# Performance work log

Measured on AMD Instinct MI355X. Metric: run time of the kernel, lower is better.

## Reference

```python
import jax, jax.numpy as jnp
import numpy as np


def _glorot(key, shape):
    lim = np.sqrt(6.0 / (shape[-2] + shape[-1])).astype(np.float32)
    return jax.random.uniform(key, shape, jnp.float32, -lim, lim)


def setup_inputs() -> dict:
    key = jax.random.key(0)
    B, F, K, L = 8192, 256, 32768, 4
    H = 2 * F          # CouplingLayer(feat_size, feat_size * 2) hidden width
    half = F // 2      # affine coupling transforms half the features
    ks = jax.random.split(key, 6)
    return {
        "inputs": jax.random.normal(ks[0], (B, F), jnp.float32),
        "W1": _glorot(ks[1], (L, half, H)),
        "b1": jnp.zeros((L, H), jnp.float32),
        "Ws": _glorot(ks[2], (L, H, half)),
        "bs": jnp.zeros((L, half), jnp.float32),
        "Wt": _glorot(ks[3], (L, H, half)),
        "bt": jnp.zeros((L, half), jnp.float32),
        "prior": _glorot(ks[4], (K, F)),  # VQ codebook, GlorotUniform init as in source
    }


def _forward_flow(x, W1, b1, Ws, bs, Wt, bt):
    """Stack of affine coupling layers; returns (y, log|det J|) per sample."""
    L = W1.shape[0]
    jac = jnp.zeros((x.shape[0],), x.dtype)
    for l in range(L):  # small fixed layer count
        xa, xb = jnp.split(x, 2, axis=1)                 # [B, F/2] each
        h = jax.nn.relu(xa @ W1[l] + b1[l])              # [B, 2F]
        s_raw = h @ Ws[l] + bs[l]                        # [B, F/2]
        s = s_raw if l == L - 1 else jnp.tanh(s_raw)     # last layer: tf.identity
        t = h @ Wt[l] + bt[l]
        yb = xb * jnp.exp(s) + t
        jac = jac + jnp.sum(s, axis=1)
        x = jnp.concatenate([yb, xa], axis=1)            # swap halves for mixing
    return x, jac


def reference(inputs, W1, b1, Ws, bs, Wt, bt, prior):
    sg = jax.lax.stop_gradient
    x, jac = _forward_flow(inputs, W1, b1, Ws, bs, Wt, bt)   # [B, F], [B]
    # pairwise squared distance to codebook: [B, K]
    na = jnp.sum(x * x, axis=1, keepdims=True)               # [B, 1]
    nb = jnp.sum(prior * prior, axis=1)[None, :]             # [1, K]
    d = jnp.maximum(na - 2.0 * (x @ prior.T) + nb, 0.0)      # [B, K]
    target_ind = jnp.argmin(d, axis=1)                       # [B]
    target = prior[target_ind]                               # gather, [B, F]
    loss_1 = jnp.mean(jnp.sum((x - sg(target)) ** 2, axis=1) / 2)
    loss_2 = jnp.mean(jnp.sum((sg(x) - target) ** 2, axis=1) / 2)
    loss = loss_1 + 0.25 * loss_2 - jnp.mean(jac)
    return x, loss
```

## Files before the change

### kernel.cpp

```cpp
#include <hip/hip_runtime.h>
#include <hip/hip_fp8.h>
#include <stdint.h>

#define NB     8192
#define NF     256
#define NHALF  128
#define NHID   512
#define NLAY   4
#define NK     32768

#define SX     (1.0f / 16.0f)
#define SP     (256.0f)

typedef __attribute__((ext_vector_type(8))) short bf16x8;
typedef __attribute__((ext_vector_type(4))) float f32x4;
typedef __attribute__((ext_vector_type(2))) long i64x2;

static __device__ __forceinline__ unsigned short f2bf(float f) {
  union { float f; unsigned int u; } v; v.f = f;
  return (unsigned short)((v.u + 0x7FFFu + ((v.u >> 16) & 1u)) >> 16);
}
static __device__ __forceinline__ float bf2f(unsigned short u) {
  union { unsigned int u; float f; } v; v.u = ((unsigned int)u) << 16; return v.f;
}
static __device__ __forceinline__ unsigned char f2fp8(float f) {
  __hip_fp8_e4m3 q(f);
  return (unsigned char)q.__x;
}
static __device__ __forceinline__ float fp82f(unsigned char b) {
  __hip_fp8_e4m3 q; q.__x = b; return (float)q;
}
static __device__ __forceinline__ int kperm(int k) {
  return ((k >> 3) & 3) * 64 + ((k >> 5) << 3) + (k & 7);
}

static __device__ __forceinline__ void load_lds16(const void* g, void* l) {
  __builtin_amdgcn_global_load_lds(
      (const __attribute__((address_space(1))) unsigned int*)g,
      (__attribute__((address_space(3))) unsigned int*)l, 16, 0, 0);
}

static __device__ __forceinline__ unsigned long long packsi(float v, int idx) {
  unsigned int b = __float_as_uint(v);
  b = (b & 0x80000000u) ? ~b : (b | 0x80000000u);
  return ((unsigned long long)b << 32) | (unsigned int)(~(unsigned int)idx);
}

static __device__ __forceinline__ float fast_tanh(float x) {
  const float xc = fminf(fmaxf(x, -15.f), 15.f);
  const float e2 = __expf(2.f * xc);
  return 1.f - 2.f / (e2 + 1.f);
}

static __device__ __forceinline__ int swadr(int kseg, int nrows, int row, int kin) {
  return (kseg * nrows + row) * 64 + (((kin >> 3) ^ (row & 7)) * 8) + (kin & 7);
}

static __device__ __forceinline__ void stage_seg(
    int g, unsigned short* dst,
    const unsigned short* __restrict__ W1T,
    const unsigned short* __restrict__ W2I,
    int wave, int lane)
{
  const int l = g / 24, s = g % 24, nc = s / 3, t = s % 3;
  if (t == 0) {
    const unsigned short* W1l = W1T + (size_t)l * (NHID * NHALF) + (size_t)nc * 64 * 128;
#pragma unroll
    for (int u = 0; u < 4; u++) {
      const int chb = (u * 4 + wave) * 64;
      const int ch = chb + lane;
      const int kseg = ch >> 9, cs = ch & 511;
      const int row = cs >> 3, cc = (cs & 7) ^ (row & 7);
      load_lds16(W1l + (size_t)row * 128 + kseg * 64 + cc * 8, dst + chb * 8);
    }
  } else {
    const unsigned short* W2l = W2I + (size_t)l * (NF * NHID) + nc * 64 + (t - 1) * 32;
#pragma unroll
    for (int u = 0; u < 4; u++) {
      const int chb = (u * 4 + wave) * 64;
      const int ch = chb + lane;
      const int row = ch >> 2;
      const int cc = (ch & 3) ^ ((row >> 1) & 3);
      load_lds16(W2l + (size_t)row * NHID + cc * 8, dst + chb * 8);
    }
  }
}

__global__ __launch_bounds__(256, 2)
void flow_all(const float* __restrict__ in,
              const unsigned short* __restrict__ W1T,
              const unsigned short* __restrict__ W2I,
              const float* __restrict__ b1A,
              const float* __restrict__ bsA,
              const float* __restrict__ btA,
              float* __restrict__ xout,
              unsigned char* __restrict__ xf8,
              float* __restrict__ jac)
{
  __shared__ __align__(16) unsigned short Xb[2][16 * 128];
  __shared__ __align__(16) unsigned short Hs[16 * 64];
  __shared__ __align__(16) unsigned short Bs[3][8192];
  __shared__ float b1s[NLAY * NHID];
  __shared__ float bss[NLAY * NHALF];
  __shared__ float bts[NLAY * NHALF];
  __shared__ float jlds[3][16];
  const int tid = threadIdx.x;
  const int lane = tid & 63, wave = tid >> 6;
  const int q = lane >> 4, c = lane & 15;
  const int m0 = blockIdx.x * 16;

  stage_seg(0, Bs[0], W1T, W2I, wave, lane);

#pragma unroll
  for (int v = 0; v < 4; v++) {
    const int t4 = tid + v * 256;
    const int row = t4 >> 6, f4 = t4 & 63;
    const float4 d = *(const float4*)(in + (size_t)(m0 + row) * NF + f4 * 4);
    unsigned short* dst = Xb[f4 >> 5];
    const int feat = (f4 & 31) * 4;
    const float vals[4] = {d.x, d.y, d.z, d.w};
#pragma unroll
    for (int u = 0; u < 4; u++) {
      const int fe = feat + u;
      dst[swadr(fe >> 6, 16, row, fe & 63)] = f2bf(vals[u]);
    }
  }

#pragma unroll
  for (int v = 0; v < 8; v++) b1s[tid + v * 256] = b1A[tid + v * 256];
#pragma unroll
  for (int v = 0; v < 2; v++) {
    bss[tid + v * 256] = bsA[tid + v * 256];
    bts[tid + v * 256] = btA[tid + v * 256];
  }

  stage_seg(1, Bs[1], W1T, W2I, wave, lane);

  float jr[4] = {0.f, 0.f, 0.f, 0.f};
  bf16x8 af1[4];
  const f32x4 z = {0.f, 0.f, 0.f, 0.f};
  f32x4 acc2[4];

  for (int gs = 0; gs < 96; gs++) {
    if (gs < 95)
      asm volatile("s_waitcnt vmcnt(4) lgkmcnt(0)\n\ts_barrier" ::: "memory");
    else
      asm volatile("s_waitcnt vmcnt(0) lgkmcnt(0)\n\ts_barrier" ::: "memory");

    if (gs + 2 < 96) stage_seg(gs + 2, Bs[(gs + 2) % 3], W1T, W2I, wave, lane);

    const int l = gs / 24, s = gs % 24, nc8 = s / 3, typ = s % 3;
    const unsigned short* B = Bs[gs % 3];
    unsigned short* XA = Xb[l & 1];
    unsigned short* XB = Xb[1 - (l & 1)];

    if (typ == 0) {
      if (s == 0) {
#pragma unroll
        for (int kw = 0; kw < 4; kw++) {
          const int kch = kw * 4 + q;
          af1[kw] = *(const bf16x8*)(XA + ((kch >> 3) * 16 + c) * 64 +
                                     (((kch & 7) ^ (c & 7)) * 8));
        }
#pragma unroll
        for (int j = 0; j < 4; j++) acc2[j] = z;
      }
      f32x4 acc1 = z;
      const int rb = wave * 16 + c;
#pragma unroll
      for (int kw = 0; kw < 4; kw++) {
        const int kseg = kw >> 1, g = (kw & 1) * 4 + q;
        const bf16x8 bf = *(const bf16x8*)(B + (kseg * 64 + rb) * 64 + ((g ^ (rb & 7)) * 8));
        acc1 = __builtin_amdgcn_mfma_f32_16x16x32_bf16(af1[kw], bf, acc1, 0, 0, 0);
      }
      const int hc = wave * 16 + c;
      const float bb = b1s[l * NHID + nc8 * 64 + hc];
#pragma unroll
      for (int r = 0; r < 4; r++) {
        float v = acc1[r] + bb;
        v = v > 0.f ? v : 0.f;
        Hs[swadr(0, 16, 4 * q + r, hc)] = f2bf(v);
      }
    } else {
      const int half = typ - 1;
      const bf16x8 afh = *(const bf16x8*)(Hs + c * 64 + (((half * 4 + q) ^ (c & 7)) * 8));
#pragma unroll
      for (int j = 0; j < 4; j++) {
        const int rb = wave * 64 + 16 * j + c;
        const bf16x8 bf = *(const bf16x8*)(B + rb * 32 + ((q ^ ((rb >> 1) & 3)) * 8));
        acc2[j] = __builtin_amdgcn_mfma_f32_16x16x32_bf16(afh, bf, acc2[j], 0, 0, 0);
      }
    }

    if (s == 23) {
      const int parity = c & 1;
      const int lastl = (l == NLAY - 1);
      const float* bsl = bss + l * NHALF;
      const float* btl = bts + l * NHALF;
#pragma unroll
      for (int j = 0; j < 4; j++) {
        const int col = wave * 64 + 16 * j + c;
#pragma unroll
        for (int r = 0; r < 4; r++) {
          const float val = acc2[j][r];
          const float oth = __shfl_xor(val, 1);
          if (!parity) {
            const int feat = col >> 1;
            float sv = val + bsl[feat];
            if (!lastl) sv = fast_tanh(sv);
            const float t = oth + btl[feat];
            const int row = 4 * q + r;
            const int xaddr = swadr(feat >> 6, 16, row, feat & 63);
            const float xb = bf2f(XB[xaddr]);
            const float yb = xb * __expf(sv) + t;
            jr[r] += sv;
            XB[xaddr] = f2bf(yb);
            if (l >= 2) {
              const int k = lastl ? feat : (NHALF + feat);
              const size_t grow = (size_t)(m0 + row) * NF;
              xout[grow + k] = yb;
              xf8[(size_t)(m0 + row) * 256 + kperm(k)] = f2fp8(yb * SX);
            }
          }
        }
      }
    }
  }

  float v0[4];
#pragma unroll
  for (int r = 0; r < 4; r++) {
    float v = jr[r];
    v += __shfl_xor(v, 1); v += __shfl_xor(v, 2);
    v += __shfl_xor(v, 4); v += __shfl_xor(v, 8);
    if (c == 0) {
      if (wave) jlds[wave - 1][4 * q + r] = v;
      else v0[r] = v;
    }
  }
  __syncthreads();
  if (wave == 0 && c == 0) {
#pragma unroll
    for (int r = 0; r < 4; r++) {
      const int row = 4 * q + r;
      jac[m0 + row] = v0[r] + jlds[0][row] + jlds[1][row] + jlds[2][row];
    }
  }
}

__global__ __launch_bounds__(256, 2)
void vq_argmax(const unsigned char* __restrict__ X8,
               const unsigned char* __restrict__ P8,
               const float* __restrict__ nbh,
               unsigned long long* __restrict__ gbest)
{
  __shared__ __align__(16) unsigned char Bs[2][64 * 256];
  const int tid = threadIdx.x;
  const int lane = tid & 63, wave = tid >> 6;
  const int y = blockIdx.x & 15;
  const int m0 = (blockIdx.x >> 4) * 256;
  const int q = lane >> 4, c = lane & 15;
  const int mw = m0 + wave * 64;

  long af[4][8];
#pragma unroll
  for (int i = 0; i < 4; i++) {
    const unsigned char* xr = X8 + (size_t)(mw + 16 * i + c) * 256 + q * 64;
#pragma unroll
    for (int kc2 = 0; kc2 < 4; kc2++) {
      const i64x2 v = *(const i64x2*)(xr + kc2 * 16);
      af[i][2 * kc2] = v.x; af[i][2 * kc2 + 1] = v.y;
    }
  }

  float bestv[16];
  int besti[16];
#pragma unroll
  for (int t = 0; t < 16; t++) { bestv[t] = -1e30f; besti[t] = 0; }

  {
    const int n0s = y * 2048;
#pragma unroll
    for (int u = 0; u < 4; u++) {
      const int chb = (u * 4 + wave) * 64;
      const int ch = chb + lane;
      const int row = ch >> 4, gslot = ch & 15;
      load_lds16(P8 + (size_t)(n0s + row) * 256 + (gslot ^ (row & 15)) * 16,
                 Bs[0] + chb * 16);
    }
  }

  for (int nt = 0; nt < 32; nt++) {
    const int n0 = y * 2048 + nt * 64;
    __syncthreads();

    float nbr[4];
#pragma unroll
    for (int j = 0; j < 4; j++) nbr[j] = nbh[n0 + 16 * j + c];

    if (nt + 1 < 32) {
      const int n0s = n0 + 64;
      unsigned char* dst = Bs[(nt + 1) & 1];
#pragma unroll
      for (int u = 0; u < 4; u++) {
        const int chb = (u * 4 + wave) * 64;
        const int ch = chb + lane;
        const int row = ch >> 4, gslot = ch & 15;
        load_lds16(P8 + (size_t)(n0s + row) * 256 + (gslot ^ (row & 15)) * 16,
                   dst + chb * 16);
      }
    }

    const unsigned char* Bt = Bs[nt & 1];
    const f32x4 z = {0.f, 0.f, 0.f, 0.f};
    f32x4 acc[4][4];
#pragma unroll
    for (int i = 0; i < 4; i++)
#pragma unroll
      for (int j = 0; j < 4; j++) acc[i][j] = z;

#pragma unroll
    for (int kc2 = 0; kc2 < 4; kc2++) {
      const int g = q * 4 + kc2;
#pragma unroll
      for (int j = 0; j < 4; j++) {
        const int rb = 16 * j + c;
        const i64x2 b2 = *(const i64x2*)(Bt + rb * 256 + ((g ^ (rb & 15)) * 16));
#pragma unroll
        for (int i = 0; i < 4; i++) {
          acc[i][j] = __builtin_amdgcn_mfma_f32_16x16x32_fp8_fp8(af[i][2 * kc2],     b2.x, acc[i][j], 0, 0, 0);
          acc[i][j] = __builtin_amdgcn_mfma_f32_16x16x32_fp8_fp8(af[i][2 * kc2 + 1], b2.y, acc[i][j], 0, 0, 0);
        }
      }
    }

#pragma unroll
    for (int j = 0; j < 4; j++) {
      const int col = n0 + 16 * j + c;
      const float nb = nbr[j];
#pragma unroll
      for (int i = 0; i < 4; i++)
#pragma unroll
        for (int r = 0; r < 4; r++) {
          const float sc = acc[i][j][r] - nb;
          const int t = i * 4 + r;
          if (sc > bestv[t]) { bestv[t] = sc; besti[t] = col; }
        }
    }
  }

#pragma unroll
  for (int t = 0; t < 16; t++) {
    float lv = bestv[t]; int li = besti[t];
#pragma unroll
    for (int mk = 8; mk >= 1; mk >>= 1) {
      const float ov = __shfl_xor(lv, mk);
      const int oi = __shfl_xor(li, mk);
      if (ov > lv || (ov == lv && oi < li)) { lv = ov; li = oi; }
    }
    if (c == 0) {
      const int row = mw + 16 * (t >> 2) + q * 4 + (t & 3);
      atomicMax(&gbest[row], packsi(lv, li));
    }
  }
}

__global__ void prep_all(const float* __restrict__ W1,
                         const float* __restrict__ Ws,
                         const float* __restrict__ Wt,
                         const float* __restrict__ prior,
                         unsigned short* __restrict__ W1T,
                         unsigned short* __restrict__ W2I,
                         unsigned char* __restrict__ p8,
                         float* __restrict__ nbh,
                         unsigned long long* __restrict__ gbest,
                         float* __restrict__ accum)
{
  __shared__ float ts[64 * 65];
  const int bx = blockIdx.x;
  const int tid = threadIdx.x;
  if (bx < 2048) {
    const int k = bx * 16 + (tid >> 4);
    const int l16 = tid & 15;
    float s = 0.f;
#pragma unroll
    for (int v = 0; v < 4; v++) {
      const int off = (v * 16 + l16) * 4;
      const float4 d = *(const float4*)(prior + (size_t)k * NF + off);
      uchar4 o;
      o.x = f2fp8(d.x * SP); o.y = f2fp8(d.y * SP);
      o.z = f2fp8(d.z * SP); o.w = f2fp8(d.w * SP);
      *(uchar4*)(p8 + (size_t)k * 256 + kperm(off)) = o;
      const float q0 = fp82f(o.x), q1 = fp82f(o.y), q2 = fp82f(o.z), q3 = fp82f(o.w);
      s += q0 * q0 + q1 * q1 + q2 * q2 + q3 * q3;
    }
#pragma unroll
    for (int mk = 8; mk >= 1; mk >>= 1) s += __shfl_xor(s, mk);
    if (l16 == 0) nbh[k] = 0.5f * s * (SX / SP);
  } else if (bx < 2112) {
    const int job = bx - 2048;
    const int l = job >> 4, t = job & 15;
    const int k0 = (t >> 3) * 64, n0 = (t & 7) * 64;
    const float* src = W1 + (size_t)l * NHALF * NHID;
#pragma unroll
    for (int v = 0; v < 16; v++) {
      const int e = tid + v * 256;
      const int kk = e >> 6, nn = e & 63;
      ts[kk * 65 + nn] = src[(size_t)(k0 + kk) * NHID + n0 + nn];
    }
    __syncthreads();
    unsigned short* dst = W1T + (size_t)l * NHID * NHALF;
#pragma unroll
    for (int v = 0; v < 16; v++) {
      const int e = tid + v * 256;
      const int nn = e >> 6, kk = e & 63;
      dst[(size_t)(n0 + nn) * NHALF + k0 + kk] = f2bf(ts[kk * 65 + nn]);
    }
  } else if (bx < 2240) {
    const int job = bx - 2112;
    const int l = job >> 5, rem = job & 31;
    const int b = rem >> 4;
    const int k0 = ((rem >> 1) & 7) * 64;
    const int f0 = (rem & 1) * 64;
    const float* src = (b ? Wt : Ws) + (size_t)l * NHID * NHALF;
#pragma unroll
    for (int v = 0; v < 16; v++) {
      const int e = tid + v * 256;
      const int kk = e >> 6, nn = e & 63;
      ts[kk * 65 + nn] = src[(size_t)(k0 + kk) * NHALF + f0 + nn];
    }
    __syncthreads();
#pragma unroll
    for (int v = 0; v < 16; v++) {
      const int e = tid + v * 256;
      const int nn = e >> 6, kk = e & 63;
      W2I[((size_t)l * NF + 2 * (f0 + nn) + b) * NHID + k0 + kk] = f2bf(ts[kk * 65 + nn]);
    }
  } else {
    const int idx = (bx - 2240) * 256 + tid;
    if (idx < NB) gbest[idx] = 0ull;
    if (idx < 4) accum[idx] = 0.f;
  }
}

__global__ void vq_finalize(const float* __restrict__ X,
                            const float* __restrict__ prior,
                            const unsigned long long* __restrict__ gbest,
                            const float* __restrict__ jac,
                            float* __restrict__ accum,
                            float* __restrict__ loss)
{
  const int wave = threadIdx.x >> 6, lane = threadIdx.x & 63;
  const int gw = blockIdx.x * 4 + wave;
  float accd = 0.f, accj = 0.f;
  for (int r = 0; r < 8; r++) {
    const int row = gw * 8 + r;
    const unsigned int idx = ~(unsigned int)(gbest[row]);
    const float* x = X + (size_t)row * NF;
    const float* p = prior + (size_t)idx * NF;
#pragma unroll
    for (int u = 0; u < 4; u++) {
      const int d = lane + u * 64;
      const float df = x[d] - p[d];
      accd += df * df;
    }
    if (lane == 0) accj += jac[row];
  }
#pragma unroll
  for (int mk = 32; mk >= 1; mk >>= 1) {
    accd += __shfl_xor(accd, mk);
    accj += __shfl_xor(accj, mk);
  }
  __shared__ float sd[4], sj[4];
  if (lane == 0) { sd[wave] = accd; sj[wave] = accj; }
  __syncthreads();
  if (threadIdx.x == 0) {
    atomicAdd(&accum[0], sd[0] + sd[1] + sd[2] + sd[3]);
    atomicAdd(&accum[1], sj[0] + sj[1] + sj[2] + sj[3]);
    __threadfence();
    const unsigned int t = atomicAdd((unsigned int*)&accum[2], 1u);
    if (t == 255u) {
      const float d = atomicAdd(&accum[0], 0.f);
      const float jv = atomicAdd(&accum[1], 0.f);
      loss[0] = 1.25f * (0.5f * d / (float)NB) - jv / (float)NB;
    }
  }
}

extern "C" void kernel_launch(void* const* d_in, const int* in_sizes, int n_in,
                              void* d_out, int out_size, void* d_ws, size_t ws_size,
                              hipStream_t stream)
{
  (void)in_sizes; (void)n_in; (void)out_size; (void)ws_size;
  const float* inputs = (const float*)d_in[0];
  const float* W1 = (const float*)d_in[1];
  const float* b1 = (const float*)d_in[2];
  const float* Ws = (const float*)d_in[3];
  const float* bs = (const float*)d_in[4];
  const float* Wt = (const float*)d_in[5];
  const float* bt = (const float*)d_in[6];
  const float* prior = (const float*)d_in[7];

  char* p = (char*)d_ws;
  auto alloc = [&](size_t bytes) { char* r = p; p += (bytes + 255) & ~(size_t)255; return r; };
  unsigned short* W1T  = (unsigned short*)alloc((size_t)NLAY * NHID * NHALF * 2);
  unsigned short* W2I  = (unsigned short*)alloc((size_t)NLAY * NF * NHID * 2);
  unsigned char* P8    = (unsigned char*)alloc((size_t)NK * 256);
  float* NBH           = (float*)alloc((size_t)NK * 4);
  unsigned char* XF8   = (unsigned char*)alloc((size_t)NB * 256);
  float* JAC           = (float*)alloc((size_t)NB * 4);
  unsigned long long* GBEST = (unsigned long long*)alloc((size_t)NB * 8);
  float* ACC           = (float*)alloc(256);

  float* xout = (float*)d_out;
  float* loss = xout + (size_t)NB * NF;

  prep_all<<<dim3(2272), 256, 0, stream>>>(
      W1, Ws, Wt, prior, W1T, W2I, P8, NBH, GBEST, ACC);

  flow_all<<<dim3(NB / 16), 256, 0, stream>>>(
      inputs, W1T, W2I, b1, bs, bt, xout, XF8, JAC);

  vq_argmax<<<dim3(32 * 16), 256, 0, stream>>>(XF8, P8, NBH, GBEST);
  vq_finalize<<<dim3(256), 256, 0, stream>>>(xout, prior, GBEST, JAC, ACC, loss);
}
```

Measured before the change: 285.7 us.

## Use scaled 16x16x128 fp8 MFMA for codebook distances and stagger weight segments

The codebook distance GEMM moves from the 16x16x32 fp8 MFMA (two per 16-byte load) to the gfx950 scaled 16x16x128 f8f6f4 MFMA with unit scales. That cuts the MFMA instruction count fourfold, and the fp8 layouts of activations and codebook drop the kperm permutation so they match the new operand layout. The negated codebook norm is folded into the accumulator init, removing one subtract per score. Separately, each flow block rotates the order of its hidden-chunk segments and swaps the output halves by block index, spreading concurrent weight reads across addresses. The risks are a wrong operand layout or scale encoding for the new instruction, which would silently change argmin results.

```diff
diff --git a/kernel.cpp b/kernel.cpp
--- a/kernel.cpp
+++ b/kernel.cpp
@@ -14,7 +14,7 @@
 
 typedef __attribute__((ext_vector_type(8))) short bf16x8;
 typedef __attribute__((ext_vector_type(4))) float f32x4;
-typedef __attribute__((ext_vector_type(2))) long i64x2;
+typedef __attribute__((ext_vector_type(8))) int i32x8;
 
 static __device__ __forceinline__ unsigned short f2bf(float f) {
   union { float f; unsigned int u; } v; v.f = f;
@@ -29,9 +29,6 @@
 }
 static __device__ __forceinline__ float fp82f(unsigned char b) {
   __hip_fp8_e4m3 q; q.__x = b; return (float)q;
-}
-static __device__ __forceinline__ int kperm(int k) {
-  return ((k >> 3) & 3) * 64 + ((k >> 5) << 3) + (k & 7);
 }
 
 static __device__ __forceinline__ void load_lds16(const void* g, void* l) {
@@ -60,9 +57,11 @@
     int g, unsigned short* dst,
     const unsigned short* __restrict__ W1T,
     const unsigned short* __restrict__ W2I,
-    int wave, int lane)
+    int wave, int lane, int bxr, int hswap)
 {
-  const int l = g / 24, s = g % 24, nc = s / 3, t = s % 3;
+  const int l = g / 24, s = g % 24;
+  const int nc = ((s / 3) + bxr) & 7;
+  const int t = s % 3;
   if (t == 0) {
     const unsigned short* W1l = W1T + (size_t)l * (NHID * NHALF) + (size_t)nc * 64 * 128;
 #pragma unroll
@@ -74,7 +73,8 @@
       load_lds16(W1l + (size_t)row * 128 + kseg * 64 + cc * 8, dst + chb * 8);
     }
   } else {
-    const unsigned short* W2l = W2I + (size_t)l * (NF * NHID) + nc * 64 + (t - 1) * 32;
+    const int half = (t - 1) ^ hswap;
+    const unsigned short* W2l = W2I + (size_t)l * (NF * NHID) + nc * 64 + half * 32;
 #pragma unroll
     for (int u = 0; u < 4; u++) {
       const int chb = (u * 4 + wave) * 64;
@@ -108,8 +108,10 @@
   const int lane = tid & 63, wave = tid >> 6;
   const int q = lane >> 4, c = lane & 15;
   const int m0 = blockIdx.x * 16;
-
-  stage_seg(0, Bs[0], W1T, W2I, wave, lane);
+  const int bxr = blockIdx.x & 7;
+  const int hswap = (blockIdx.x >> 3) & 1;
+
+  stage_seg(0, Bs[0], W1T, W2I, wave, lane, bxr, hswap);
 
 #pragma unroll
   for (int v = 0; v < 4; v++) {
@@ -134,7 +136,7 @@
     bts[tid + v * 256] = btA[tid + v * 256];
   }
 
-  stage_seg(1, Bs[1], W1T, W2I, wave, lane);
+  stage_seg(1, Bs[1], W1T, W2I, wave, lane, bxr, hswap);
 
   float jr[4] = {0.f, 0.f, 0.f, 0.f};
   bf16x8 af1[4];
@@ -147,9 +149,10 @@
     else
       asm volatile("s_waitcnt vmcnt(0) lgkmcnt(0)\n\ts_barrier" ::: "memory");
 
-    if (gs + 2 < 96) stage_seg(gs + 2, Bs[(gs + 2) % 3], W1T, W2I, wave, lane);
-
-    const int l = gs / 24, s = gs % 24, nc8 = s / 3, typ = s % 3;
+    if (gs + 2 < 96) stage_seg(gs + 2, Bs[(gs + 2) % 3], W1T, W2I, wave, lane, bxr, hswap);
+
+    const int l = gs / 24, s = gs % 24, typ = s % 3;
+    const int nc8 = ((s / 3) + bxr) & 7;
     const unsigned short* B = Bs[gs % 3];
     unsigned short* XA = Xb[l & 1];
     unsigned short* XB = Xb[1 - (l & 1)];
@@ -182,7 +185,7 @@
         Hs[swadr(0, 16, 4 * q + r, hc)] = f2bf(v);
       }
     } else {
-      const int half = typ - 1;
+      const int half = (typ - 1) ^ hswap;
       const bf16x8 afh = *(const bf16x8*)(Hs + c * 64 + (((half * 4 + q) ^ (c & 7)) * 8));
 #pragma unroll
       for (int j = 0; j < 4; j++) {
@@ -219,7 +222,7 @@
               const int k = lastl ? feat : (NHALF + feat);
               const size_t grow = (size_t)(m0 + row) * NF;
               xout[grow + k] = yb;
-              xf8[(size_t)(m0 + row) * 256 + kperm(k)] = f2fp8(yb * SX);
+              xf8[(size_t)(m0 + row) * 256 + k] = f2fp8(yb * SX);
             }
           }
         }
@@ -261,15 +264,17 @@
   const int m0 = (blockIdx.x >> 4) * 256;
   const int q = lane >> 4, c = lane & 15;
   const int mw = m0 + wave * 64;
-
-  long af[4][8];
+  const int one = 0x7F7F7F7F;
+
+  i32x8 af[4][2];
 #pragma unroll
   for (int i = 0; i < 4; i++) {
-    const unsigned char* xr = X8 + (size_t)(mw + 16 * i + c) * 256 + q * 64;
-#pragma unroll
-    for (int kc2 = 0; kc2 < 4; kc2++) {
-      const i64x2 v = *(const i64x2*)(xr + kc2 * 16);
-      af[i][2 * kc2] = v.x; af[i][2 * kc2 + 1] = v.y;
+    const unsigned char* xr = X8 + (size_t)(mw + 16 * i + c) * 256 + q * 32;
+#pragma unroll
+    for (int h = 0; h < 2; h++) {
+      const int4 lo = *(const int4*)(xr + h * 128);
+      const int4 hi = *(const int4*)(xr + h * 128 + 16);
+      af[i][h] = (i32x8){lo.x, lo.y, lo.z, lo.w, hi.x, hi.y, hi.z, hi.w};
     }
   }
 
@@ -312,37 +317,36 @@
     }
 
     const unsigned char* Bt = Bs[nt & 1];
-    const f32x4 z = {0.f, 0.f, 0.f, 0.f};
     f32x4 acc[4][4];
 #pragma unroll
     for (int i = 0; i < 4; i++)
 #pragma unroll
-      for (int j = 0; j < 4; j++) acc[i][j] = z;
-
-#pragma unroll
-    for (int kc2 = 0; kc2 < 4; kc2++) {
-      const int g = q * 4 + kc2;
-#pragma unroll
-      for (int j = 0; j < 4; j++) {
-        const int rb = 16 * j + c;
-        const i64x2 b2 = *(const i64x2*)(Bt + rb * 256 + ((g ^ (rb & 15)) * 16));
-#pragma unroll
-        for (int i = 0; i < 4; i++) {
-          acc[i][j] = __builtin_amdgcn_mfma_f32_16x16x32_fp8_fp8(af[i][2 * kc2],     b2.x, acc[i][j], 0, 0, 0);
-          acc[i][j] = __builtin_amdgcn_mfma_f32_16x16x32_fp8_fp8(af[i][2 * kc2 + 1], b2.y, acc[i][j], 0, 0, 0);
-        }
+      for (int j = 0; j < 4; j++)
+        acc[i][j] = (f32x4){-nbr[j], -nbr[j], -nbr[j], -nbr[j]};
+
+#pragma unroll
+    for (int j = 0; j < 4; j++) {
+      const unsigned char* base = Bt + (16 * j + c) * 256;
+#pragma unroll
+      for (int h = 0; h < 2; h++) {
+        const int4 b0 = *(const int4*)(base + ((8 * h + 2 * q)     ^ c) * 16);
+        const int4 b1 = *(const int4*)(base + ((8 * h + 2 * q + 1) ^ c) * 16);
+        const i32x8 bf = (i32x8){b0.x, b0.y, b0.z, b0.w, b1.x, b1.y, b1.z, b1.w};
+#pragma unroll
+        for (int i = 0; i < 4; i++)
+          acc[i][j] = __builtin_amdgcn_mfma_scale_f32_16x16x128_f8f6f4(
+              af[i][h], bf, acc[i][j], 0, 0, 0, one, 0, one);
       }
     }
 
 #pragma unroll
     for (int j = 0; j < 4; j++) {
       const int col = n0 + 16 * j + c;
-      const float nb = nbr[j];
 #pragma unroll
       for (int i = 0; i < 4; i++)
 #pragma unroll
         for (int r = 0; r < 4; r++) {
-          const float sc = acc[i][j][r] - nb;
+          const float sc = acc[i][j][r];
           const int t = i * 4 + r;
           if (sc > bestv[t]) { bestv[t] = sc; besti[t] = col; }
         }
@@ -390,7 +394,7 @@
       uchar4 o;
       o.x = f2fp8(d.x * SP); o.y = f2fp8(d.y * SP);
       o.z = f2fp8(d.z * SP); o.w = f2fp8(d.w * SP);
-      *(uchar4*)(p8 + (size_t)k * 256 + kperm(off)) = o;
+      *(uchar4*)(p8 + (size_t)k * 256 + off) = o;
       const float q0 = fp82f(o.x), q1 = fp82f(o.y), q2 = fp82f(o.z), q3 = fp82f(o.w);
       s += q0 * q0 + q1 * q1 + q2 * q2 + q3 * q3;
     }
```

New measurement: 259.4 us. 9.2% less time.
